# Optimization experiments

Measured on AMD Instinct MI355X. Metric: run time of the kernel, lower is better.

The kernel has to match this reference:

```python
import jax, jax.numpy as jnp
import numpy as np

T, B, IN, H, E = 100, 1, 36, 256, 2048


def setup_inputs() -> dict:
    key = jax.random.key(0)
    ks = jax.random.split(key, 18)
    rn = lambda k, shape, s=1.0: jax.random.normal(k, shape, jnp.float32) * s
    return dict(
        Y=rn(ks[0], (T, B, IN)),
        h0=rn(ks[1], (1, B, H)),
        c0=rn(ks[2], (1, B, H)),
        outEncoder=rn(ks[3], (E, H), 0.1),
        W_ih=rn(ks[4], (4 * H, IN), 0.1),
        W_hh=rn(ks[5], (4 * H, H), 0.1),
        b_ih=rn(ks[6], (4 * H,), 0.1),
        b_hh=rn(ks[7], (4 * H,), 0.1),
        att_W=rn(ks[8], (H, H), 0.1),
        att_V=rn(ks[9], (H, H), 0.1),
        att_b=rn(ks[10], (H, 1), 0.1),
        att_vector=rn(ks[11], (1, H), 0.1),
        W1=rn(ks[12], (H, 2 * H), 0.1),
        b1=rn(ks[13], (H,), 0.1),
        W2=rn(ks[14], (H, H), 0.1),
        b2=rn(ks[15], (H,), 0.1),
        W3=rn(ks[16], (IN, H), 0.1),
        b3=rn(ks[17], (IN,), 0.1),
    )


def reference(Y, h0, c0, outEncoder, W_ih, W_hh, b_ih, b_hh,
              att_W, att_V, att_b, att_vector, W1, b1, W2, b2, W3, b3):
    h = jnp.squeeze(h0, 0)  # [B,H]
    c = jnp.squeeze(c0, 0)  # [B,H]
    # VOut = att_V @ outEncoder^T is timestep-invariant: precompute. [H,E]
    VOut = att_V @ outEncoder.T

    def step(carry, y):
        h, c = carry  # h: [B,H], c: [B,H] (context from prev step after step 0)
        gates = y @ W_ih.T + b_ih + h @ W_hh.T + b_hh  # [B,4H]
        i_g, f_g, g_g, o_g = jnp.split(gates, 4, axis=1)
        cLSTM = jax.nn.sigmoid(f_g) * c + jax.nn.sigmoid(i_g) * jnp.tanh(g_g)
        h_new = jax.nn.sigmoid(o_g) * jnp.tanh(cLSTM)  # [B,H]
        # additive attention: hidden expanded to every encoder position
        WS = att_W @ h_new.T  # [H,1], broadcasts over E columns
        Escore = jnp.tanh(WS + VOut + att_b)  # [H,E]
        scores = att_vector @ Escore  # [1,E]
        alpha = jax.nn.softmax(scores, axis=-1)  # [1,E]
        ctx = alpha @ outEncoder  # [1,H]
        # MLP on concat(new cell state, context)
        v = jnp.concatenate([cLSTM, ctx], axis=1)  # [1,2H]
        v = jax.nn.relu(v @ W1.T + b1)
        v = jax.nn.relu(v @ W2.T + b2)
        out = v @ W3.T + b3  # [1,36]
        # NB: original feeds the attention context back as the LSTM cell state
        return (h_new, ctx), out

    (_, c_final), outputs = jax.lax.scan(step, (h, c), Y)
    return outputs, c_final  # outputs: [100,1,36]
```

## Files before the change

kernel.cpp:

```cpp
#include <hip/hip_runtime.h>
#include <stdint.h>


static constexpr float    L2E = 1.44269504088896341f;
static constexpr float    K2  = 2.88539008177792681f;
static constexpr unsigned SPIN_LIMIT = 200000u;
static constexpr int      FSTRIDE = 16;

static constexpr size_t OFF_BC   = 0;
static constexpr size_t OFF_YG   = 524288;
static constexpr size_t OFF_GRAW = 626688;
static constexpr size_t OFF_CRAW = 729088;
static constexpr size_t CRAW_CP  = 25600;
static constexpr size_t OFF_STOT = 831488;
static constexpr size_t OFF_V1   = 857216;
static constexpr size_t OFF_V2   = 882816;
static constexpr size_t OFF_SYNC = 908416;

__device__ __forceinline__ float exp2fast(float x){ return __builtin_amdgcn_exp2f(x); }
__device__ __forceinline__ float rcpfast(float x){ return __builtin_amdgcn_rcpf(x); }
__device__ __forceinline__ float sigf(float x){ return rcpfast(1.f + exp2fast(-x*L2E)); }
__device__ __forceinline__ float tanhfast(float x){
  float E = exp2fast(x*K2);
  return 1.f - 2.f*rcpfast(E + 1.f);
}
__device__ __forceinline__ unsigned short f2bf(float f){
  unsigned b = __float_as_uint(f);
  return (unsigned short)((b + 0x7FFFu + ((b>>16)&1u))>>16);
}
__device__ __forceinline__ float bf2f(unsigned short u){ return __uint_as_float(((unsigned)u)<<16); }

__device__ __forceinline__ void gstore(float* p, float v){
  __hip_atomic_store(p, v, __ATOMIC_RELAXED, __HIP_MEMORY_SCOPE_AGENT);
}
__device__ __forceinline__ float gload(const float* p){
  return __hip_atomic_load(p, __ATOMIC_RELAXED, __HIP_MEMORY_SCOPE_AGENT);
}
__device__ __forceinline__ void gstore_u32(unsigned* p, unsigned v){
  __hip_atomic_store(p, v, __ATOMIC_RELAXED, __HIP_MEMORY_SCOPE_AGENT);
}
__device__ __forceinline__ unsigned gload_u32(const unsigned* p){
  return __hip_atomic_load(p, __ATOMIC_RELAXED, __HIP_MEMORY_SCOPE_AGENT);
}
__device__ __forceinline__ void gatomic_addf(float* p, float v){
  (void)__hip_atomic_fetch_add(p, v, __ATOMIC_RELAXED, __HIP_MEMORY_SCOPE_AGENT);
}

__device__ __forceinline__ void fbar(unsigned* flags, int w, unsigned ep){
  asm volatile("s_waitcnt vmcnt(0)" ::: "memory");
  __syncthreads();
  if (threadIdx.x == 0) gstore_u32(&flags[w*FSTRIDE], ep);
  if (threadIdx.x < 64) {
    int lane = threadIdx.x;
    unsigned it = 0;
    for (;;) {
      unsigned v = (lane < 32) ? gload_u32(&flags[lane*FSTRIDE]) : ep;
      if (__all((int)(v >= ep))) break;
      __builtin_amdgcn_s_sleep(1);
      if (++it > SPIN_LIMIT) break;
    }
  }
  __syncthreads();
}
__device__ __forceinline__ void fwait_sleep(unsigned* flags, unsigned ep){
  if (threadIdx.x < 64) {
    int lane = threadIdx.x;
    unsigned it = 0;
    for (;;) {
      unsigned v = (lane < 32) ? gload_u32(&flags[lane*FSTRIDE]) : ep;
      if (__all((int)(v >= ep))) break;
      __builtin_amdgcn_s_sleep(2);
      if (++it > SPIN_LIMIT) break;
    }
  }
  __syncthreads();
}
__device__ __forceinline__ void arrive_cnt(unsigned* cnt){
  asm volatile("s_waitcnt vmcnt(0)" ::: "memory");
  __syncthreads();
  if (threadIdx.x == 0)
    __hip_atomic_fetch_add(cnt, 1u, __ATOMIC_RELAXED, __HIP_MEMORY_SCOPE_AGENT);
}
__device__ __forceinline__ void poll_ge(unsigned* p, unsigned tgt){
  if (threadIdx.x == 0){
    unsigned it = 0;
    while (gload_u32(p) < tgt){
      __builtin_amdgcn_s_sleep(2);
      if (++it > SPIN_LIMIT) break;
    }
  }
  __syncthreads();
}

__global__ __launch_bounds__(256) void rnn_prep(
    const float* __restrict__ Y, const float* __restrict__ h0,
    const float* __restrict__ outE, const float* __restrict__ W_ih,
    const float* __restrict__ W_hh, const float* __restrict__ b_ih,
    const float* __restrict__ b_hh, const float* __restrict__ att_V,
    const float* __restrict__ att_b, float* __restrict__ ws)
{
  __shared__ float avT[32*257];
  __shared__ float oeL[8*257];
  __shared__ float yL[40];
  __shared__ float h0L[256];
  const int b = blockIdx.x, tid = threadIdx.x;
  float* ws_bc   = ws + OFF_BC;
  float* ws_yg   = ws + OFF_YG;
  float* ws_graw = ws + OFF_GRAW;

  if (b < 256) {
    int e0 = b*8;
    for (int r=0;r<8;r++) oeL[r*257 + tid] = outE[(size_t)(e0+r)*256 + tid];
    int hl = tid & 31, er = tid >> 5;
    for (int ht=0; ht<8; ++ht) {
      __syncthreads();
      for (int i=0;i<32;i++){ int lin = tid + i*256; int r = lin>>8, j = lin&255;
        avT[r*257 + j] = att_V[(size_t)(ht*32+r)*256 + j]; }
      __syncthreads();
      float acc = 0.f;
      for (int j=0;j<256;j++) acc = fmaf(avT[hl*257 + j], oeL[er*257 + j], acc);
      int h = ht*32 + hl;
      ws_bc[(size_t)(e0+er)*256 + h] = (acc + att_b[h]) * K2;
    }
  } else if (b < 260) {
    int g = b - 256;
    for (int u=0; u<25; ++u) {
      int t = g*25 + u;
      __syncthreads();
      if (tid < 36) yL[tid] = Y[t*36 + tid];
      __syncthreads();
      for (int q=0;q<4;q++){
        int i = tid + 256*q;
        float acc = b_ih[i] + b_hh[i];
        for (int j=0;j<36;j++) acc = fmaf(W_ih[(size_t)i*36 + j], yL[j], acc);
        ws_yg[(size_t)t*1024 + i] = acc;
      }
    }
  } else if (b < 292) {
    int s = b - 260;
    if (tid < 256) h0L[tid] = h0[tid];
    if (tid < 36)  yL[tid]  = Y[tid];
    __syncthreads();
    int r = tid>>3, l8 = tid&7;
    int R = s*32 + r;
    float acc = 0.f;
    for (int q=0;q<32;q++){ int j = l8*32 + q; acc = fmaf(W_hh[(size_t)R*256 + j], h0L[j], acc); }
    acc += __shfl_xor(acc,1); acc += __shfl_xor(acc,2); acc += __shfl_xor(acc,4);
    if (l8 == 0){
      float full = acc + b_ih[R] + b_hh[R];
      for (int j=0;j<36;j++) full = fmaf(W_ih[(size_t)R*36 + j], yL[j], full);
      ws_graw[R] = full;
    }
  } else if (b == 292) {
    unsigned* s0 = (unsigned*)(ws + OFF_SYNC);
    #pragma unroll
    for (int k=0;k<4;k++) gstore_u32(&s0[tid + k*256], 0u);
  } else if (b == 293) {
    if (tid < 128) gstore(&ws[OFF_STOT + tid], 0.f);
  } else {
    int t = b - 294;
    #pragma unroll
    for (int c=0;c<4;c++)
      gstore(&ws[OFF_CRAW + (size_t)c*CRAW_CP + (size_t)t*256 + tid], 0.f);
  }
}

__global__ __launch_bounds__(512, 2) void rnn_main(
    const float* __restrict__ c0, const float* __restrict__ outE,
    const float* __restrict__ W_hh, const float* __restrict__ att_W,
    const float* __restrict__ att_vec,
    const float* __restrict__ W1, const float* __restrict__ b1,
    const float* __restrict__ W2, const float* __restrict__ b2,
    const float* __restrict__ W3, const float* __restrict__ b3,
    float* __restrict__ out, float* __restrict__ ws)
{
  __shared__ __align__(16) unsigned char smem[140288];
  const int w = blockIdx.x;
  const int tid = threadIdx.x;

  float* ws_yg    = ws + OFF_YG;
  float* ws_graw  = ws + OFF_GRAW;
  float* ws_craw  = ws + OFF_CRAW;
  float* ws_stot  = ws + OFF_STOT;
  float* ws_v1    = ws + OFF_V1;
  float* ws_v2    = ws + OFF_V2;
  unsigned* flags = (unsigned*)(ws + OFF_SYNC);
  unsigned* fv1   = flags + 512;
  unsigned* fv2   = flags + 768;

  if (w < 32) {
    float*          bcS    = (float*)(smem);
    unsigned short* oeS    = (unsigned short*)(smem + 67584);
    float*          whhS   = (float*)(smem + 100352);
    float*          wsS    = (float*)(smem + 133632);
    float*          hS     = (float*)(smem + 134688);
    float*          scoreS = (float*)(smem + 135712);
    float*          wexpS  = (float*)(smem + 135968);
    float*          pS     = (float*)(smem + 136224);
    float*          avS    = (float*)(smem + 138272);

    unsigned awP[64];
    { int r = tid>>1, p = tid&1;
      const float* arow = att_W + (size_t)r*256 + p*128;
      #pragma unroll
      for (int q=0;q<64;q++){
        unsigned lo = f2bf(arow[2*q]);
        unsigned hi = f2bf(arow[2*q+1]);
        awP[q] = lo | (hi<<16);
      } }
    float Vpart = 0.f;
    { int l8 = tid & 7;
      #pragma unroll
      for (int k=0;k<32;k++) Vpart += att_vec[l8*32 + k]; }

    const float* ws_bc = ws + OFF_BC;
    for (int i=0;i<32;i++){ int lin = tid + i*512; int col = lin>>8, h = lin&255;
      bcS[col*264 + h + (h>>5)] = ws_bc[(size_t)(w*64+col)*256 + h]; }
    for (int i=0;i<32;i++){ int lin = tid + i*512; int col = lin>>8, h = lin&255;
      oeS[col*256 + h] = f2bf(outE[(size_t)(w*64+col)*256 + h]); }
    for (int i=0;i<16;i++){ int lin = tid + i*512; int r = lin>>8, j = lin&255;
      whhS[r*260 + j] = W_hh[(size_t)(w*32+r)*256 + j]; }
    if (tid < 256) avS[tid + (tid>>5)] = -2.f * att_vec[tid];
    __syncthreads();

    for (int t = 0; t < 100; ++t) {
      float ig, fg, gg, og;
      float cr0, cr1, cr2, cr3, st;
      if (tid < 256) {
        const float* g = ws_graw + (size_t)t*1024;
        ig = gload(&g[tid]);     fg = gload(&g[256+tid]);
        gg = gload(&g[512+tid]); og = gload(&g[768+tid]);
        if (t > 0) {
          const float* cb = ws_craw + (size_t)(t-1)*256 + tid;
          cr0 = gload(cb);             cr1 = gload(cb + CRAW_CP);
          cr2 = gload(cb + 2*CRAW_CP); cr3 = gload(cb + 3*CRAW_CP);
          st  = gload(&ws_stot[t-1]);
        }
      }
      if (tid < 256) {
        float c;
        if (t == 0) c = c0[tid];
        else        c = ((cr0+cr1)+(cr2+cr3)) * rcpfast(st);
        float cl = sigf(fg)*c + sigf(ig)*tanhfast(gg);
        float hn = sigf(og)*tanhfast(cl);
        hS[tid] = hn;
      }
      __syncthreads();
      { int r = tid>>1, p = tid&1;
        const float4* h4 = (const float4*)(hS + p*128);
        float acc = 0.f;
        #pragma unroll
        for (int i=0;i<32;i++){
          float4 hv = h4[i];
          unsigned pk0 = awP[2*i], pk1 = awP[2*i+1];
          acc = fmaf(__uint_as_float(pk0<<16),           hv.x, acc);
          acc = fmaf(__uint_as_float(pk0 & 0xffff0000u), hv.y, acc);
          acc = fmaf(__uint_as_float(pk1<<16),           hv.z, acc);
          acc = fmaf(__uint_as_float(pk1 & 0xffff0000u), hv.w, acc);
        }
        acc += __shfl_xor(acc, 1);
        if (p == 0) wsS[r + (r>>5)] = acc * K2; }
      __syncthreads();
      { int col = tid >> 3, l8 = tid & 7;
        const float* bcR = bcS + col*264 + l8*33;
        const float* wsR = wsS + l8*33;
        const float* avR = avS + l8*33;
        float acc = Vpart;
        #pragma unroll
        for (int k=0;k<32;k++){
          float E = exp2fast(bcR[k] + wsR[k]);
          acc = fmaf(avR[k], rcpfast(E + 1.f), acc);
        }
        acc += __shfl_xor(acc,1); acc += __shfl_xor(acc,2); acc += __shfl_xor(acc,4);
        if (l8 == 0) scoreS[col] = acc; }
      __syncthreads();
      if (tid < 64) {
        float ev = exp2fast(scoreS[tid] * L2E);
        wexpS[tid] = ev;
        float s = ev;
        #pragma unroll
        for (int d=1; d<64; d<<=1) s += __shfl_xor(s, d);
        if (tid == 0) gatomic_addf(&ws_stot[t], s);
      }
      __syncthreads();
      { int h = tid & 255, half = tid >> 8;
        float accp = 0.f;
        #pragma unroll
        for (int i=0;i<32;i++){ int lc = half*32 + i;
          accp = fmaf(wexpS[lc], bf2f(oeS[lc*256 + h]), accp); }
        pS[half*256 + h] = accp; }
      __syncthreads();
      if (tid < 256)
        gatomic_addf(&ws_craw[(size_t)(w>>3)*CRAW_CP + (size_t)t*256 + tid],
                     pS[tid] + pS[256 + tid]);
      if (t <= 98) {
        int r32 = tid >> 4, l16 = tid & 15;
        float acc2 = 0.f;
        #pragma unroll
        for (int q=0;q<16;q++){ int j = l16 + 16*q; acc2 = fmaf(whhS[r32*260 + j], hS[j], acc2); }
        acc2 += __shfl_xor(acc2,1); acc2 += __shfl_xor(acc2,2);
        acc2 += __shfl_xor(acc2,4); acc2 += __shfl_xor(acc2,8);
        if (l16 == 0){ int R = w*32 + r32;
          gstore(&ws_graw[(size_t)(t+1)*1024 + R], acc2 + ws_yg[(size_t)(t+1)*1024 + R]); }
      }
      fbar(flags, w, (unsigned)(t+1));
    }
    if (w == 0 && tid < 256) {
      const float* cb = ws_craw + (size_t)99*256 + tid;
      float rsum = (gload(cb) + gload(cb + CRAW_CP))
                 + (gload(cb + 2*CRAW_CP) + gload(cb + 3*CRAW_CP));
      out[3600 + tid] = rsum * rcpfast(gload(&ws_stot[99]));
    }
  } else if (w < 36) {
    float* wmS = (float*)(smem);
    float* vbS = (float*)(smem + 133632);
    int m = w - 32;
    for (int i=0;i<64;i++){ int lin = tid + i*512; int r = lin>>9, k = lin&511;
      wmS[r*520 + k + (k>>6)] = W1[(size_t)(m*64+r)*512 + k]; }
    __syncthreads();
    for (int s=0; s<100; ++s){
      fwait_sleep(flags, (unsigned)(s+1));
      { float val;
        if (tid < 256) {
          const float* g = ws_graw + (size_t)s*1024;
          float ig = gload(&g[tid]);     float fg = gload(&g[256+tid]);
          float gg = gload(&g[512+tid]);
          float c;
          if (s == 0) c = c0[tid];
          else {
            const float* cb = ws_craw + (size_t)(s-1)*256 + tid;
            float a0 = gload(cb);             float a1 = gload(cb + CRAW_CP);
            float a2 = gload(cb + 2*CRAW_CP); float a3 = gload(cb + 3*CRAW_CP);
            c = ((a0+a1)+(a2+a3)) * rcpfast(gload(&ws_stot[s-1]));
          }
          val = sigf(fg)*c + sigf(ig)*tanhfast(gg);
        } else {
          const float* cb = ws_craw + (size_t)s*256 + (tid-256);
          float rsum = (gload(cb) + gload(cb + CRAW_CP))
                     + (gload(cb + 2*CRAW_CP) + gload(cb + 3*CRAW_CP));
          val = rsum * rcpfast(gload(&ws_stot[s]));
        }
        vbS[tid + (tid>>6)] = val; }
      __syncthreads();
      int row = tid >> 3, l8 = tid & 7;
      const float* wr = wmS + row*520 + l8*65;
      const float* vr = vbS + l8*65;
      float acc = 0.f;
      #pragma unroll
      for (int q=0;q<64;q++) acc = fmaf(wr[q], vr[q], acc);
      acc += __shfl_xor(acc,1); acc += __shfl_xor(acc,2); acc += __shfl_xor(acc,4);
      if (l8 == 0){ int i = m*64 + row; gstore(&ws_v1[(size_t)s*256 + i], fmaxf(acc + b1[i], 0.f)); }
      arrive_cnt(&fv1[s]);
      __syncthreads();
    }
  } else if (w < 38) {
    float* wmS = (float*)(smem);
    float* vbS = (float*)(smem + 133632);
    int m = w - 36;
    for (int i=0;i<64;i++){ int lin = tid + i*512; int r = lin>>8, k = lin&255;
      wmS[r*260 + k + (k>>6)] = W2[(size_t)(m*128+r)*256 + k]; }
    __syncthreads();
    for (int s=0; s<100; ++s){
      poll_ge(&fv1[s], 4u);
      if (tid < 256) vbS[tid + (tid>>6)] = gload(&ws_v1[(size_t)s*256 + tid]);
      __syncthreads();
      int row = tid >> 2, l4 = tid & 3;
      const float* wr = wmS + row*260 + l4*65;
      const float* vr = vbS + l4*65;
      float acc = 0.f;
      #pragma unroll
      for (int q=0;q<64;q++) acc = fmaf(wr[q], vr[q], acc);
      acc += __shfl_xor(acc,1); acc += __shfl_xor(acc,2);
      if (l4 == 0){ int i = m*128 + row; gstore(&ws_v2[(size_t)s*256 + i], fmaxf(acc + b2[i], 0.f)); }
      arrive_cnt(&fv2[s]);
      __syncthreads();
    }
  } else {
    float* wmS = (float*)(smem);
    float* vbS = (float*)(smem + 37440);
    for (int lin = tid; lin < 36*256; lin += 512){ int r = lin>>8, k = lin&255;
      wmS[r*260 + k + (k>>6)] = W3[(size_t)r*256 + k]; }
    __syncthreads();
    for (int s=0; s<100; ++s){
      poll_ge(&fv2[s], 2u);
      if (tid < 256) vbS[tid + (tid>>6)] = gload(&ws_v2[(size_t)s*256 + tid]);
      __syncthreads();
      if (tid < 288) {
        int row = tid >> 3, l8 = tid & 7;
        int kb = l8*32;
        const float* wr = wmS + row*260 + kb + (kb>>6);
        const float* vr = vbS + kb + (kb>>6);
        float acc = 0.f;
        #pragma unroll
        for (int q=0;q<32;q++) acc = fmaf(wr[q], vr[q], acc);
        acc += __shfl_xor(acc,1); acc += __shfl_xor(acc,2); acc += __shfl_xor(acc,4);
        if (l8 == 0) out[s*36 + row] = acc + b3[row];
      }
      __syncthreads();
    }
  }
}

extern "C" void kernel_launch(void* const* d_in, const int* in_sizes, int n_in,
                              void* d_out, int out_size, void* d_ws, size_t ws_size,
                              hipStream_t stream) {
  (void)in_sizes; (void)n_in; (void)out_size; (void)ws_size;
  const float* Y       = (const float*)d_in[0];
  const float* h0      = (const float*)d_in[1];
  const float* c0      = (const float*)d_in[2];
  const float* outEnc  = (const float*)d_in[3];
  const float* W_ih    = (const float*)d_in[4];
  const float* W_hh    = (const float*)d_in[5];
  const float* b_ih    = (const float*)d_in[6];
  const float* b_hh    = (const float*)d_in[7];
  const float* att_W   = (const float*)d_in[8];
  const float* att_V   = (const float*)d_in[9];
  const float* att_b   = (const float*)d_in[10];
  const float* att_vec = (const float*)d_in[11];
  const float* W1      = (const float*)d_in[12];
  const float* b1      = (const float*)d_in[13];
  const float* W2      = (const float*)d_in[14];
  const float* b2      = (const float*)d_in[15];
  const float* W3      = (const float*)d_in[16];
  const float* b3      = (const float*)d_in[17];
  float* out = (float*)d_out;
  float* ws  = (float*)d_ws;

  rnn_prep<<<dim3(394), dim3(256), 0, stream>>>(Y, h0, outEnc, W_ih, W_hh, b_ih, b_hh,
                                                att_V, att_b, ws);
  rnn_main<<<dim3(39), dim3(512), 0, stream>>>(c0, outEnc, W_hh, att_W, att_vec,
                                               W1, b1, W2, b2, W3, b3, out, ws);
}
```

Before: 643.4 us.

## Split softmax-context and recurrent matvec across thread halves, drop two barriers

In the per-timestep loop of the attention blocks, the first 256 threads now compute exp weights, the weighted encoder sum and the weight total in one pass, without the separate wexp/pS shared buffers. This removes two __syncthreads and the partial-sum staging. The other 256 threads run the W_hh recurrent matvec for the next step at the same time, with yg prefetched early. Each context thread now does 64 serial iterations and recomputes the 64 exponentials redundantly, which lengthens the critical path of that half.

```diff
diff --git a/kernel.cpp b/kernel.cpp
--- a/kernel.cpp
+++ b/kernel.cpp
@@ -195,8 +195,6 @@
     float*          wsS    = (float*)(smem + 133632);
     float*          hS     = (float*)(smem + 134688);
     float*          scoreS = (float*)(smem + 135712);
-    float*          wexpS  = (float*)(smem + 135968);
-    float*          pS     = (float*)(smem + 136224);
     float*          avS    = (float*)(smem + 138272);
 
     unsigned awP[64];
@@ -226,6 +224,8 @@
     for (int t = 0; t < 100; ++t) {
       float ig, fg, gg, og;
       float cr0, cr1, cr2, cr3, st;
+      float ygn = 0.f;
+      int   gr32 = (tid - 256) >> 3, gl8 = tid & 7;
       if (tid < 256) {
         const float* g = ws_graw + (size_t)t*1024;
         ig = gload(&g[tid]);     fg = gload(&g[256+tid]);
@@ -236,6 +236,8 @@
           cr2 = gload(cb + 2*CRAW_CP); cr3 = gload(cb + 3*CRAW_CP);
           st  = gload(&ws_stot[t-1]);
         }
+      } else if (t <= 98 && gl8 == 0) {
+        ygn = ws_yg[(size_t)(t+1)*1024 + w*32 + gr32];
       }
       if (tid < 256) {
         float c;
@@ -274,34 +276,24 @@
         acc += __shfl_xor(acc,1); acc += __shfl_xor(acc,2); acc += __shfl_xor(acc,4);
         if (l8 == 0) scoreS[col] = acc; }
       __syncthreads();
-      if (tid < 64) {
-        float ev = exp2fast(scoreS[tid] * L2E);
-        wexpS[tid] = ev;
-        float s = ev;
+      if (tid < 256) {
+        const unsigned short* oeC = oeS + tid;
+        float accp = 0.f, sw = 0.f;
         #pragma unroll
-        for (int d=1; d<64; d<<=1) s += __shfl_xor(s, d);
-        if (tid == 0) gatomic_addf(&ws_stot[t], s);
-      }
-      __syncthreads();
-      { int h = tid & 255, half = tid >> 8;
-        float accp = 0.f;
-        #pragma unroll
-        for (int i=0;i<32;i++){ int lc = half*32 + i;
-          accp = fmaf(wexpS[lc], bf2f(oeS[lc*256 + h]), accp); }
-        pS[half*256 + h] = accp; }
-      __syncthreads();
-      if (tid < 256)
-        gatomic_addf(&ws_craw[(size_t)(w>>3)*CRAW_CP + (size_t)t*256 + tid],
-                     pS[tid] + pS[256 + tid]);
-      if (t <= 98) {
-        int r32 = tid >> 4, l16 = tid & 15;
+        for (int lc=0; lc<64; ++lc){
+          float ev = exp2fast(scoreS[lc] * L2E);
+          sw += ev;
+          accp = fmaf(ev, bf2f(oeC[lc*256]), accp);
+        }
+        gatomic_addf(&ws_craw[(size_t)(w>>3)*CRAW_CP + (size_t)t*256 + tid], accp);
+        if (tid == 0) gatomic_addf(&ws_stot[t], sw);
+      } else if (t <= 98) {
         float acc2 = 0.f;
         #pragma unroll
-        for (int q=0;q<16;q++){ int j = l16 + 16*q; acc2 = fmaf(whhS[r32*260 + j], hS[j], acc2); }
-        acc2 += __shfl_xor(acc2,1); acc2 += __shfl_xor(acc2,2);
-        acc2 += __shfl_xor(acc2,4); acc2 += __shfl_xor(acc2,8);
-        if (l16 == 0){ int R = w*32 + r32;
-          gstore(&ws_graw[(size_t)(t+1)*1024 + R], acc2 + ws_yg[(size_t)(t+1)*1024 + R]); }
+        for (int q=0;q<32;q++){ int j = gl8 + 8*q; acc2 = fmaf(whhS[gr32*260 + j], hS[j], acc2); }
+        acc2 += __shfl_xor(acc2,1); acc2 += __shfl_xor(acc2,2); acc2 += __shfl_xor(acc2,4);
+        if (gl8 == 0)
+          gstore(&ws_graw[(size_t)(t+1)*1024 + w*32 + gr32], acc2 + ygn);
       }
       fbar(flags, w, (unsigned)(t+1));
     }
```

New measurement: 773.4 us. 1.2x slower.
